# Performance work log

Measured on AMD Instinct MI355X. Metric: run time of the kernel, lower is better.

Reference implementation:

```python
import jax, jax.numpy as jnp
import numpy as np

V_THRESH = 0.3

@jax.custom_vjp
def spike(x):
    return (x > 0).astype(x.dtype)

def _spike_fwd(x):
    return spike(x), x

def _spike_bwd(x, g):
    # rectangular straight-through surrogate gradient (pass grad where |x| < 0.5)
    return (g * (jnp.abs(x) < 0.5).astype(g.dtype),)

spike.defvjp(_spike_fwd, _spike_bwd)


def setup_inputs() -> dict:
    key = jax.random.key(0)
    B, T, H = 128, 2048, 128
    k1, = jax.random.split(key, 1)
    x_seq = jax.random.normal(k1, (B, T, H), dtype=jnp.float32)
    v0 = jnp.zeros((B, H), dtype=jnp.float32)
    z0 = jnp.zeros((B, H), dtype=jnp.float32)
    decay_raw = jnp.zeros((H,), dtype=jnp.float32)  # nn.initializers.constant(0.0)
    return {"x_seq": x_seq, "v0": v0, "z0": z0, "decay_raw": decay_raw}


def reference(x_seq, v0, z0, decay_raw):
    # LIF recurrence: v_t = v_{t-1} * decay * (1 - z_{t-1}) + x_t ; z_t = spike(v_t - v_thresh)
    decay = jax.nn.sigmoid(decay_raw)  # (H,)

    def step(carry, x_t):
        v, z = carry
        v = v * decay * (1.0 - z) + x_t
        z_out = spike(v - V_THRESH)
        return (v, z_out), z_out

    x_tb = jnp.swapaxes(x_seq, 0, 1)  # [T, B, H] for lax.scan over time
    (_, _), spk_tb = jax.lax.scan(step, (v0, z0), x_tb)
    return jnp.swapaxes(spk_tb, 0, 1)  # [B, T, H]
```

## Files before the change

### kernel.cpp

```cpp
#include <hip/hip_runtime.h>
#include <math.h>


constexpr int Bdim = 128;
constexpr int Tdim = 2048;
constexpr int Hdim = 128;
constexpr int HW   = 64;
constexpr int U    = 128;
constexpr float VTH = 0.3f;

typedef const __attribute__((address_space(1))) void* gptr_t;
typedef __attribute__((address_space(3))) void* lptr_t;

__global__ __launch_bounds__(64) void lif_kernel(
    const float* __restrict__ x,
    const float* __restrict__ v0,
    const float* __restrict__ z0,
    const float* __restrict__ decay_raw,
    float* __restrict__ out)
{
    __shared__ float lds[2][U][HW];

    const int lane = threadIdx.x;
    const int w  = blockIdx.x;
    const int b  = w >> 1;
    const int h0 = (w & 1) * HW;
    const int h  = h0 + lane;

    const float decay = 1.0f / (1.0f + expf(-decay_raw[h]));
    float v = v0[b * Hdim + h];
    float z = z0[b * Hdim + h];

    const float* xbase = x   + (size_t)b * Tdim * Hdim + h0;
    float*       obase = out + (size_t)b * Tdim * Hdim + h0 + lane;

    const int sub_r = lane >> 4;
    const int sub_c = (lane & 15) * 4;

    auto issue_tile = [&](int t0, int buf) {
        const float* g = xbase + (size_t)t0 * Hdim + sub_c + (size_t)sub_r * Hdim;
        #pragma unroll
        for (int j = 0; j < U / 4; ++j) {
            __builtin_amdgcn_global_load_lds(
                (gptr_t)(const void*)(g + (size_t)(4 * j) * Hdim),
                (lptr_t)(void*)&lds[buf][4 * j][0],
                16, 0, 0);
        }
    };

    issue_tile(0, 0);
    __syncthreads();

    int buf = 0;
    for (int tc = 0; tc < Tdim; tc += U) {
        if (tc + U < Tdim) issue_tile(tc + U, buf ^ 1);

        float* op = obase + (size_t)tc * Hdim;
        #pragma unroll 16
        for (int tl = 0; tl < U; ++tl) {
            const float xv = lds[buf][tl][lane];
            const float vd = v * decay;
            v = ((z > 0.5f) ? 0.0f : vd) + xv;
            z = (v > VTH) ? 1.0f : 0.0f;
            op[(size_t)tl * Hdim] = z;
        }

        __syncthreads();
        buf ^= 1;
    }
}

extern "C" void kernel_launch(void* const* d_in, const int* in_sizes, int n_in,
                              void* d_out, int out_size, void* d_ws, size_t ws_size,
                              hipStream_t stream) {
    const float* x         = (const float*)d_in[0];
    const float* v0        = (const float*)d_in[1];
    const float* z0        = (const float*)d_in[2];
    const float* decay_raw = (const float*)d_in[3];
    float* out = (float*)d_out;

    lif_kernel<<<Bdim * Hdim / HW, 64, 0, stream>>>(x, v0, z0, decay_raw, out);
}
```

Before: 248.0 us.

## Warp-specialize LIF kernel: one compute wave, helper waves load and store tiles

Each block grows from one wave to eight. Wave 0 runs the serial recurrence and writes spikes back into the LDS tile in place. The other waves prefetch input tiles two ahead through a 4-deep LDS ring, then flush finished tiles to global memory with float4 stores. This takes the strided per-timestep global stores and load issue off the latency-bound serial wave. In exchange it uses 128KB of LDS per block, which limits occupancy, and adds a block barrier per tile.

```diff
diff --git a/kernel.cpp b/kernel.cpp
--- a/kernel.cpp
+++ b/kernel.cpp
@@ -7,67 +7,87 @@
 constexpr int Hdim = 128;
 constexpr int HW   = 64;
 constexpr int U    = 128;
+constexpr int NBUF = 4;
+constexpr int NW   = 8;
+constexpr int NTILE = Tdim / U;
 constexpr float VTH = 0.3f;
 
 typedef const __attribute__((address_space(1))) void* gptr_t;
 typedef __attribute__((address_space(3))) void* lptr_t;
 
-__global__ __launch_bounds__(64) void lif_kernel(
+__global__ __launch_bounds__(NW * 64) void lif_kernel(
     const float* __restrict__ x,
     const float* __restrict__ v0,
     const float* __restrict__ z0,
     const float* __restrict__ decay_raw,
     float* __restrict__ out)
 {
-    __shared__ float lds[2][U][HW];
+    __shared__ float lds[NBUF][U][HW];
 
-    const int lane = threadIdx.x;
-    const int w  = blockIdx.x;
-    const int b  = w >> 1;
-    const int h0 = (w & 1) * HW;
-    const int h  = h0 + lane;
-
-    const float decay = 1.0f / (1.0f + expf(-decay_raw[h]));
-    float v = v0[b * Hdim + h];
-    float z = z0[b * Hdim + h];
+    const int tid  = threadIdx.x;
+    const int wave = tid >> 6;
+    const int lane = tid & 63;
+    const int blk  = blockIdx.x;
+    const int b    = blk >> 1;
+    const int h0   = (blk & 1) * HW;
 
     const float* xbase = x   + (size_t)b * Tdim * Hdim + h0;
-    float*       obase = out + (size_t)b * Tdim * Hdim + h0 + lane;
+    float*       obase = out + (size_t)b * Tdim * Hdim + h0;
 
-    const int sub_r = lane >> 4;
-    const int sub_c = (lane & 15) * 4;
+    const int sub = (lane >> 4) * Hdim + (lane & 15) * 4;
 
-    auto issue_tile = [&](int t0, int buf) {
-        const float* g = xbase + (size_t)t0 * Hdim + sub_c + (size_t)sub_r * Hdim;
+    auto fill = [&](int tile, int buf) {
+        const float* g = xbase + (size_t)tile * U * Hdim + sub;
         #pragma unroll
-        for (int j = 0; j < U / 4; ++j) {
+        for (int q = 0; q < 4; ++q) {
+            const int jj = wave * 4 + q;
             __builtin_amdgcn_global_load_lds(
-                (gptr_t)(const void*)(g + (size_t)(4 * j) * Hdim),
-                (lptr_t)(void*)&lds[buf][4 * j][0],
+                (gptr_t)(const void*)(g + (size_t)(4 * jj) * Hdim),
+                (lptr_t)(void*)&lds[buf][4 * jj][0],
                 16, 0, 0);
         }
     };
 
-    issue_tile(0, 0);
+    auto flush = [&](int tile, int buf) {
+        #pragma unroll
+        for (int q = 0; q < 4; ++q) {
+            const int s   = wave * 4 + q;
+            const int row = 4 * s + (lane >> 4);
+            const int col = (lane & 15) * 4;
+            const float4 vv = *(const float4*)&lds[buf][row][col];
+            *(float4*)(obase + (size_t)(tile * U + row) * Hdim + col) = vv;
+        }
+    };
+
+    float decay = 0.f, v = 0.f, z = 0.f;
+    if (wave == 0) {
+        decay = 1.0f / (1.0f + expf(-decay_raw[h0 + lane]));
+        v = v0[b * Hdim + h0 + lane];
+        z = z0[b * Hdim + h0 + lane];
+    }
+
+    fill(0, 0);
+    fill(1, 1);
     __syncthreads();
 
-    int buf = 0;
-    for (int tc = 0; tc < Tdim; tc += U) {
-        if (tc + U < Tdim) issue_tile(tc + U, buf ^ 1);
+    for (int k = 0; k < NTILE; ++k) {
+        if (k + 2 < NTILE) fill(k + 2, (k + 2) % NBUF);
+        if (k >= 1)        flush(k - 1, (k - 1) % NBUF);
 
-        float* op = obase + (size_t)tc * Hdim;
-        #pragma unroll 16
-        for (int tl = 0; tl < U; ++tl) {
-            const float xv = lds[buf][tl][lane];
-            const float vd = v * decay;
-            v = ((z > 0.5f) ? 0.0f : vd) + xv;
-            z = (v > VTH) ? 1.0f : 0.0f;
-            op[(size_t)tl * Hdim] = z;
+        if (wave == 0) {
+            const int cb = k % NBUF;
+            #pragma unroll 16
+            for (int tl = 0; tl < U; ++tl) {
+                const float xv = lds[cb][tl][lane];
+                const float vd = v * decay;
+                v = ((z > 0.5f) ? 0.0f : vd) + xv;
+                z = (v > VTH) ? 1.0f : 0.0f;
+                lds[cb][tl][lane] = z;
+            }
         }
-
         __syncthreads();
-        buf ^= 1;
     }
+    flush(NTILE - 1, (NTILE - 1) % NBUF);
 }
 
 extern "C" void kernel_launch(void* const* d_in, const int* in_sizes, int n_in,
@@ -79,5 +99,5 @@
     const float* decay_raw = (const float*)d_in[3];
     float* out = (float*)d_out;
 
-    lif_kernel<<<Bdim * Hdim / HW, 64, 0, stream>>>(x, v0, z0, decay_raw, out);
+    lif_kernel<<<Bdim * Hdim / HW, NW * 64, 0, stream>>>(x, v0, z0, decay_raw, out);
 }
```

Measured after the change: 240.8 us. -2.9%, faster.
